# Kernel tuning notes

Hardware: AMD Instinct MI355X
Metric: run time of the kernel (lower is better)

The kernel has to match this reference:

```python
import jax, jax.numpy as jnp
import numpy as np

OUTPUT_BUDGET = 2048
PADDING_IDX = 0
BIG = 1e9
B, TG, M = 4, 32768, 4
N_ENT, N_REL, D = 100000, 512, 128
N_RULES = 64


def setup_inputs() -> dict:
    key = jax.random.key(0)
    ks = jax.random.split(key, 8)
    # entity ids in [1, N_ENT) so padding_idx=0 is reserved
    subj = jax.random.randint(ks[0], (B, TG, M), 1, N_ENT)
    pred = jax.random.randint(ks[1], (B, TG, M), 0, N_REL)
    obj = jax.random.randint(ks[2], (B, TG, M), 1, N_ENT)
    body = jnp.stack([subj, pred, obj], axis=-1)  # [B, TG, M, 3]
    pad = jax.random.uniform(ks[3], (B, TG, M)) < 0.25
    body = body.at[..., 0].set(jnp.where(pad, PADDING_IDX, body[..., 0]))
    mask = jax.random.uniform(ks[4], (B, TG)) < 0.9  # [B, TG] bool
    rule_idx = jax.random.randint(ks[5], (B, TG), 0, N_RULES)
    ent_emb = jax.random.normal(ks[6], (N_ENT, D), dtype=jnp.float32) * 0.1
    rel_emb = jax.random.normal(ks[7], (N_REL, D), dtype=jnp.float32) * 0.1
    return {"body": body, "mask": mask, "rule_idx": rule_idx,
            "ent_emb": ent_emb, "rel_emb": rel_emb}


def reference(body, mask, rule_idx, ent_emb, rel_emb):
    # KGE (DistMult) atom scoring: gather embeddings, tri-linear dot per atom
    s = ent_emb[body[..., 0]]   # [B, TG, M, D]
    r = rel_emb[body[..., 1]]   # [B, TG, M, D]
    o = ent_emb[body[..., 2]]   # [B, TG, M, D]
    atom_scores = jnp.einsum('btmd,btmd,btmd->btm', s, r, o)  # [B, TG, M]
    body_active = body[..., 0] != PADDING_IDX
    atom_scores = jnp.where(body_active, atom_scores, BIG)
    # min-conjunction over atoms, mask inactive groundings
    scores = jnp.min(atom_scores, axis=-1)            # [B, TG]
    scores = jnp.where(mask, scores, -BIG)
    # top-k select per batch row
    top_scores, top_idx = jax.lax.top_k(scores, OUTPUT_BUDGET)  # [B, K]
    body_sel = jnp.take_along_axis(body, top_idx[:, :, None, None], axis=1)  # [B, K, M, 3]
    mask_sel = jnp.take_along_axis(mask, top_idx, axis=1)        # [B, K]
    rule_sel = jnp.take_along_axis(rule_idx, top_idx, axis=1)    # [B, K]
    return body_sel, mask_sel, rule_sel, top_scores
```

## Files before the change

kernel.cpp:

```cpp
#include <hip/hip_runtime.h>
#include <hip/hip_bf16.h>
#include <hip/hip_fp16.h>
#include <stdint.h>

constexpr int B_    = 4;
constexpr int TG_   = 32768;
constexpr int D_    = 128;
constexpr int KOUT_ = 2048;
constexpr int NH_   = 4096;
constexpr int CAPL_ = 8192;
constexpr long ENTQ_ = 100000L * D_ / 4;
constexpr long RELQ_ = 512L * D_ / 4;
#define BIGF 1e9f

#define WS_KEYS(ws)   ((unsigned long long*)(ws))
#define WS_KEYS2(ws)  ((unsigned long long*)((char*)(ws) + (1u << 20)))
#define WS_GHIST(ws)  ((uint32_t*)((char*)(ws) + (2u << 20)))
#define WS_CHSCAN(ws) ((unsigned short*)((char*)(ws) + (2u << 20) + 65536u))
#define WS_REL8(ws)   ((unsigned char*)((char*)(ws) + (3u << 20)))
#define WS_ENT8(ws)   ((unsigned char*)((char*)(ws) + (3u << 20) + 65536u))

__device__ __forceinline__ uint32_t f2u_asc(float f) {
  uint32_t b = __float_as_uint(f);
  return (b & 0x80000000u) ? ~b : (b | 0x80000000u);
}
__device__ __forceinline__ float u2f_asc(uint32_t u) {
  uint32_t b = (u & 0x80000000u) ? (u & 0x7FFFFFFFu) : ~u;
  return __uint_as_float(b);
}

__device__ __forceinline__ bool mask_is_i32(const void* mask_raw) {
  const uint32_t* mw = (const uint32_t*)mask_raw;
  bool i32 = true;
  #pragma unroll
  for (int j = 0; j < 16; ++j) i32 &= (mw[j] <= 1u);
  return i32;
}
__device__ __forceinline__ int read_mask(const void* mask_raw, int idx, bool i32) {
  return i32 ? ((const int*)mask_raw)[idx]
             : (int)((const unsigned char*)mask_raw)[idx];
}

__device__ __forceinline__ uint32_t f2e5m2(float x) {
  uint32_t u = (uint32_t)__half_as_ushort(__float2half(x));
  return (u + 0x7Fu + ((u >> 8) & 1u)) >> 8;
}

__global__ __launch_bounds__(256) void convert_kernel(
    const float* __restrict__ ent, const float* __restrict__ rel,
    unsigned char* __restrict__ ent8, unsigned char* __restrict__ rel8) {
  long stride = (long)gridDim.x * 256;
  for (long q = (long)blockIdx.x * 256 + threadIdx.x; q < ENTQ_ + RELQ_; q += stride) {
    bool isEnt = (q < ENTQ_);
    long qq = isEnt ? q : (q - ENTQ_);
    float4 v = isEnt ? ((const float4*)ent)[qq] : ((const float4*)rel)[qq];
    uint32_t b = f2e5m2(v.x) | (f2e5m2(v.y) << 8) | (f2e5m2(v.z) << 16) | (f2e5m2(v.w) << 24);
    if (isEnt) ((uint32_t*)ent8)[qq] = b;
    else       ((uint32_t*)rel8)[qq] = b;
  }
}

__device__ __forceinline__ void expand4(uint32_t w, uint32_t& lo, uint32_t& hi) {
  lo = ((w << 8) & 0xFF00u)  | ((w << 16) & 0xFF000000u);
  hi = ((w >> 8) & 0xFF00u)  | (w & 0xFF000000u);
}

__device__ __forceinline__ float dot8_e5(uint32_t sx, uint32_t sy,
                                         uint32_t rx, uint32_t ry,
                                         uint32_t ox, uint32_t oy) {
  uint32_t sw[4], rw[4], ow[4];
  expand4(sx, sw[0], sw[1]); expand4(sy, sw[2], sw[3]);
  expand4(rx, rw[0], rw[1]); expand4(ry, rw[2], rw[3]);
  expand4(ox, ow[0], ow[1]); expand4(oy, ow[2], ow[3]);
  const __half2* sh = (const __half2*)sw;
  const __half2* rh = (const __half2*)rw;
  const __half2* oh = (const __half2*)ow;
  __half2 acc = __half2{__ushort_as_half(0), __ushort_as_half(0)};
  #pragma unroll
  for (int c = 0; c < 4; ++c)
    acc = __hfma2(__hmul2(sh[c], rh[c]), oh[c], acc);
  return __low2float(acc) + __high2float(acc);
}

__device__ __forceinline__ float dot16_e5(const uint4& s, const uint4& r, const uint4& o) {
  return dot8_e5(s.x, s.y, r.x, r.y, o.x, o.y)
       + dot8_e5(s.z, s.w, r.z, r.w, o.z, o.w);
}

__global__ __launch_bounds__(256, 4) void score_e5m2_kernel(
    const int* __restrict__ body, const void* __restrict__ mask,
    const unsigned char* __restrict__ ent8, const unsigned char* __restrict__ rel8,
    unsigned long long* __restrict__ keys, uint32_t* __restrict__ ghist) {
  if (blockIdx.x < 64) ghist[blockIdx.x * 256 + threadIdx.x] = 0;
  int lane = threadIdx.x & 63;
  int wv   = threadIdx.x >> 6;
  int wid0 = blockIdx.x * 32 + wv * 8;
  int g    = lane >> 3;
  int sl   = lane & 7;
  int wid  = wid0 + g;
  const uint4* bq = (const uint4*)(body + (long)wid * 12);
  uint4 b0 = bq[0], b1 = bq[1], b2 = bq[2];
  int sI[4] = {(int)b0.x, (int)b0.w, (int)b1.z, (int)b2.y};
  int rI[4] = {(int)b0.y, (int)b1.x, (int)b1.w, (int)b2.z};
  int oI[4] = {(int)b0.z, (int)b1.y, (int)b2.x, (int)b2.w};
  bool pd[4];
  #pragma unroll
  for (int a = 0; a < 4; ++a) {
    pd[a] = (sI[a] == 0);
    if (pd[a]) { rI[a] = 0; oI[a] = 0; }
  }
  uint4 S[4], R[4], O[4];
  #pragma unroll
  for (int a = 0; a < 4; ++a) {
    S[a] = ((const uint4*)(ent8 + (long)sI[a] * D_))[sl];
    R[a] = ((const uint4*)(rel8 + (long)rI[a] * D_))[sl];
    O[a] = ((const uint4*)(ent8 + (long)oI[a] * D_))[sl];
  }
  float q[4];
  #pragma unroll
  for (int a = 0; a < 4; ++a) q[a] = dot16_e5(S[a], R[a], O[a]);
  #pragma unroll
  for (int a = 0; a < 4; ++a) {
    q[a] += __shfl_xor(q[a], 1);
    q[a] += __shfl_xor(q[a], 2);
    q[a] += __shfl_xor(q[a], 4);
    q[a] = pd[a] ? BIGF : q[a];
  }
  float m = fminf(fminf(q[0], q[1]), fminf(q[2], q[3]));
  float sc = read_mask(mask, wid, mask_is_i32(mask)) ? m : -BIGF;
  if (sl == 0) {
    uint32_t dk = ~f2u_asc(sc);
    keys[wid] = ((unsigned long long)dk << 32) | (uint32_t)(wid & (TG_ - 1));
  }
}

__global__ __launch_bounds__(1024) void histsort_kernel(
    const unsigned long long* __restrict__ keys, uint32_t* __restrict__ ghist,
    unsigned short* __restrict__ chscan, unsigned long long* __restrict__ keys2) {
  __shared__ uint32_t lh[NH_];
  __shared__ uint32_t lb[NH_];
  __shared__ unsigned long long srt[2048];
  __shared__ uint32_t wexc[16];
  int row   = blockIdx.x >> 4;
  int chunk = blockIdx.x & 15;
  int tid = threadIdx.x, lane = tid & 63, wv = tid >> 6;
  const unsigned long long* kk = keys + (long)row * TG_ + chunk * 2048;
  #pragma unroll
  for (int i = 0; i < NH_ / 1024; ++i) { lh[tid + i*1024] = 0; lb[tid + i*1024] = 0; }
  __syncthreads();
  unsigned long long k0 = kk[tid], k1 = kk[tid + 1024];
  atomicAdd(&lh[(uint32_t)(k0 >> 52)], 1u);
  atomicAdd(&lh[(uint32_t)(k1 >> 52)], 1u);
  __syncthreads();
  uint32_t* gh = ghist + row * NH_;
  #pragma unroll
  for (int i = 0; i < NH_ / 1024; ++i) {
    uint32_t v = lh[tid + i * 1024];
    if (v) atomicAdd(&gh[tid + i * 1024], v);
  }
  uint32_t c0 = lh[4*tid], c1 = lh[4*tid+1], c2 = lh[4*tid+2], c3 = lh[4*tid+3];
  uint32_t s = c0 + c1 + c2 + c3;
  uint32_t inc = s;
  #pragma unroll
  for (int off = 1; off < 64; off <<= 1) {
    uint32_t t = __shfl_up(inc, off, 64);
    if (lane >= off) inc += t;
  }
  if (lane == 63) wexc[wv] = inc;
  __syncthreads();
  if (tid < 16) {
    uint32_t v = wexc[tid], iv = v;
    #pragma unroll
    for (int off = 1; off < 16; off <<= 1) {
      uint32_t t = __shfl_up(iv, off, 64);
      if (tid >= off) iv += t;
    }
    wexc[tid] = iv - v;
  }
  __syncthreads();
  uint32_t excl = wexc[wv] + inc - s;
  uint32_t e0 = excl, e1 = e0 + c0, e2 = e1 + c1, e3 = e2 + c2, incl = e3 + c3;
  unsigned short* gc = chscan + ((long)row * 16 + chunk) * NH_;
  ushort4 sv; sv.x = (unsigned short)e1; sv.y = (unsigned short)e2;
  sv.z = (unsigned short)e3; sv.w = (unsigned short)incl;
  ((ushort4*)gc)[tid] = sv;
  lh[4*tid] = e0; lh[4*tid+1] = e1; lh[4*tid+2] = e2; lh[4*tid+3] = e3;
  __syncthreads();
  uint32_t p0 = lh[(uint32_t)(k0 >> 52)] + atomicAdd(&lb[(uint32_t)(k0 >> 52)], 1u);
  srt[p0] = k0;
  uint32_t p1 = lh[(uint32_t)(k1 >> 52)] + atomicAdd(&lb[(uint32_t)(k1 >> 52)], 1u);
  srt[p1] = k1;
  __syncthreads();
  unsigned long long* k2 = keys2 + ((long)row * 16 + chunk) * 2048;
  ((uint4*)k2)[tid] = ((const uint4*)srt)[tid];
}

__global__ __launch_bounds__(1024) void finish_kernel(
    const unsigned long long* __restrict__ keys2, const uint32_t* __restrict__ ghist,
    const unsigned short* __restrict__ chscan,
    const int* __restrict__ body, const void* __restrict__ mask,
    const int* __restrict__ rule, float* __restrict__ out) {
  __shared__ uint32_t ofs[NH_];
  __shared__ uint32_t bofs[NH_];
  __shared__ unsigned long long cand[CAPL_];
  __shared__ uint32_t wexc[16];
  __shared__ uint32_t s_th;
  int tid  = threadIdx.x;
  int lane = tid & 63;
  int wv   = tid >> 6;
  int b    = blockIdx.x;
  const uint32_t* gh = ghist + b * NH_;
  uint4 cq = ((const uint4*)gh)[tid];
  uint32_t c0 = cq.x, c1 = cq.y, c2 = cq.z, c3 = cq.w;
  #pragma unroll
  for (int i = 0; i < NH_ / 1024; ++i) bofs[tid + i * 1024] = 0;
  uint32_t s = c0 + c1 + c2 + c3;
  uint32_t inc = s;
  #pragma unroll
  for (int off = 1; off < 64; off <<= 1) {
    uint32_t t = __shfl_up(inc, off, 64);
    if (lane >= off) inc += t;
  }
  if (lane == 63) wexc[wv] = inc;
  __syncthreads();
  if (tid < 16) {
    uint32_t v = wexc[tid], iv = v;
    #pragma unroll
    for (int off = 1; off < 16; off <<= 1) {
      uint32_t t = __shfl_up(iv, off, 64);
      if (tid >= off) iv += t;
    }
    wexc[tid] = iv - v;
  }
  __syncthreads();
  uint32_t excl = wexc[wv] + inc - s;
  uint32_t e0 = excl, e1 = e0 + c0, e2 = e1 + c1, e3 = e2 + c2, incl = e3 + c3;
  if (excl < (uint32_t)KOUT_ && incl >= (uint32_t)KOUT_) {
    uint32_t t4 = (uint32_t)tid * 4;
    s_th = (e1 >= (uint32_t)KOUT_) ? t4
         : (e2 >= (uint32_t)KOUT_) ? t4 + 1
         : (e3 >= (uint32_t)KOUT_) ? t4 + 2 : t4 + 3;
  }
  ofs[4*tid] = e0; ofs[4*tid+1] = e1; ofs[4*tid+2] = e2; ofs[4*tid+3] = e3;
  __syncthreads();
  uint32_t th = s_th;
  uint32_t cnt = (uint32_t)chscan[((long)b * 16 + wv) * NH_ + th];
  const unsigned long long* k2 = keys2 + ((long)b * 16 + wv) * 2048;
  for (uint32_t i = lane; i < cnt; i += 64) {
    unsigned long long key = k2[i];
    uint32_t pfx = (uint32_t)(key >> 52);
    uint32_t pos = ofs[pfx] + atomicAdd(&bofs[pfx], 1u);
    if (pos < (uint32_t)CAPL_) cand[pos] = key;
  }
  __syncthreads();
  uint32_t n = (th + 1 < (uint32_t)NH_) ? ofs[th + 1] : (uint32_t)TG_;
  if (n > (uint32_t)CAPL_) n = CAPL_;
  bool mi32 = mask_is_i32(mask);
  for (uint32_t slot = tid; slot < n; slot += 1024) {
    unsigned long long my = cand[slot];
    uint32_t pfx = (uint32_t)(my >> 52);
    uint32_t s0 = ofs[pfx];
    uint32_t s1 = (pfx + 1 < (uint32_t)NH_) ? ofs[pfx + 1] : n;
    if (s1 > n) s1 = n;
    uint32_t r = s0;
    for (uint32_t i = s0; i < s1; ++i) r += (cand[i] < my);
    if (r >= (uint32_t)KOUT_) continue;
    int t = (int)(my & 0xFFFFFFFFu);
    float sc = u2f_asc(~(uint32_t)(my >> 32));
    int g = b * TG_ + t;
    int idx = b * KOUT_ + (int)r;
    const int* at = body + (long)g * 12;
    float* ob = out + (long)idx * 12;
    #pragma unroll
    for (int c = 0; c < 12; ++c) ob[c] = (float)at[c];
    const int base1 = B_ * KOUT_ * 12;
    out[base1 + idx]                  = read_mask(mask, g, mi32) ? 1.0f : 0.0f;
    out[base1 + B_ * KOUT_ + idx]     = (float)rule[g];
    out[base1 + 2 * B_ * KOUT_ + idx] = sc;
  }
}

extern "C" void kernel_launch(void* const* d_in, const int* in_sizes, int n_in,
                              void* d_out, int out_size, void* d_ws, size_t ws_size,
                              hipStream_t stream) {
  const int*  body = (const int*)d_in[0];
  const void* mask = d_in[1];
  const int*  rule = (const int*)d_in[2];
  const float* ent = (const float*)d_in[3];
  const float* rel = (const float*)d_in[4];
  float* out = (float*)d_out;

  unsigned long long* keys  = WS_KEYS(d_ws);
  unsigned long long* keys2 = WS_KEYS2(d_ws);
  uint32_t*       ghist  = WS_GHIST(d_ws);
  unsigned short* chscan = WS_CHSCAN(d_ws);
  unsigned char*  ent8   = WS_ENT8(d_ws);
  unsigned char*  rel8   = WS_REL8(d_ws);

  convert_kernel<<<2048, 256, 0, stream>>>(ent, rel, ent8, rel8);
  score_e5m2_kernel<<<(B_ * TG_) / 32, 256, 0, stream>>>(body, mask, ent8, rel8, keys, ghist);
  histsort_kernel<<<B_ * 16, 1024, 0, stream>>>(keys, ghist, chscan, keys2);
  finish_kernel<<<B_, 1024, 0, stream>>>(keys2, ghist, chscan, body, mask, rule, out);
}
```

Measured before the change: 66.91 us.

## Fuse histogram sort and finish kernels using last-block completion counter

Merges the per-chunk histogram sort kernel and the per-row finish kernel into one launch. Each block bumps a per-row atomic counter after writing its sorted chunk, and the last block of each row runs the threshold selection and output gather. This removes one kernel launch and its dependency gap, at the cost of larger LDS use per block (the candidate buffer) and a threadfence/atomic handshake. The counter is reset in the scoring kernel.

After: 92.27 us. +37.9%, slower.

```diff
diff --git a/kernel.cpp b/kernel.cpp
--- a/kernel.cpp
+++ b/kernel.cpp
@@ -17,6 +17,7 @@
 #define WS_KEYS2(ws)  ((unsigned long long*)((char*)(ws) + (1u << 20)))
 #define WS_GHIST(ws)  ((uint32_t*)((char*)(ws) + (2u << 20)))
 #define WS_CHSCAN(ws) ((unsigned short*)((char*)(ws) + (2u << 20) + 65536u))
+#define WS_GDONE(ws)  ((uint32_t*)((char*)(ws) + (2u << 20) + 655360u))
 #define WS_REL8(ws)   ((unsigned char*)((char*)(ws) + (3u << 20)))
 #define WS_ENT8(ws)   ((unsigned char*)((char*)(ws) + (3u << 20) + 65536u))
 
@@ -90,8 +91,10 @@
 __global__ __launch_bounds__(256, 4) void score_e5m2_kernel(
     const int* __restrict__ body, const void* __restrict__ mask,
     const unsigned char* __restrict__ ent8, const unsigned char* __restrict__ rel8,
-    unsigned long long* __restrict__ keys, uint32_t* __restrict__ ghist) {
+    unsigned long long* __restrict__ keys, uint32_t* __restrict__ ghist,
+    uint32_t* __restrict__ gdone) {
   if (blockIdx.x < 64) ghist[blockIdx.x * 256 + threadIdx.x] = 0;
+  if (blockIdx.x == 64 && threadIdx.x < B_) gdone[threadIdx.x] = 0;
   int lane = threadIdx.x & 63;
   int wv   = threadIdx.x >> 6;
   int wid0 = blockIdx.x * 32 + wv * 8;
@@ -134,13 +137,18 @@
   }
 }
 
-__global__ __launch_bounds__(1024) void histsort_kernel(
+__global__ __launch_bounds__(1024) void histsort_finish_kernel(
     const unsigned long long* __restrict__ keys, uint32_t* __restrict__ ghist,
-    unsigned short* __restrict__ chscan, unsigned long long* __restrict__ keys2) {
+    unsigned short* __restrict__ chscan, unsigned long long* __restrict__ keys2,
+    uint32_t* __restrict__ gdone,
+    const int* __restrict__ body, const void* __restrict__ mask,
+    const int* __restrict__ rule, float* __restrict__ out) {
   __shared__ uint32_t lh[NH_];
   __shared__ uint32_t lb[NH_];
   __shared__ unsigned long long srt[2048];
+  __shared__ unsigned long long cand[CAPL_];
   __shared__ uint32_t wexc[16];
+  __shared__ uint32_t s_th, s_last;
   int row   = blockIdx.x >> 4;
   int chunk = blockIdx.x & 15;
   int tid = threadIdx.x, lane = tid & 63, wv = tid >> 6;
@@ -191,31 +199,22 @@
   uint32_t p1 = lh[(uint32_t)(k1 >> 52)] + atomicAdd(&lb[(uint32_t)(k1 >> 52)], 1u);
   srt[p1] = k1;
   __syncthreads();
-  unsigned long long* k2 = keys2 + ((long)row * 16 + chunk) * 2048;
-  ((uint4*)k2)[tid] = ((const uint4*)srt)[tid];
-}
-
-__global__ __launch_bounds__(1024) void finish_kernel(
-    const unsigned long long* __restrict__ keys2, const uint32_t* __restrict__ ghist,
-    const unsigned short* __restrict__ chscan,
-    const int* __restrict__ body, const void* __restrict__ mask,
-    const int* __restrict__ rule, float* __restrict__ out) {
-  __shared__ uint32_t ofs[NH_];
-  __shared__ uint32_t bofs[NH_];
-  __shared__ unsigned long long cand[CAPL_];
-  __shared__ uint32_t wexc[16];
-  __shared__ uint32_t s_th;
-  int tid  = threadIdx.x;
-  int lane = tid & 63;
-  int wv   = tid >> 6;
-  int b    = blockIdx.x;
-  const uint32_t* gh = ghist + b * NH_;
+  unsigned long long* k2o = keys2 + ((long)row * 16 + chunk) * 2048;
+  ((uint4*)k2o)[tid] = ((const uint4*)srt)[tid];
+
+  __threadfence();
+  __syncthreads();
+  if (tid == 0) s_last = (atomicAdd(&gdone[row], 1u) == 15u) ? 1u : 0u;
+  __syncthreads();
+  if (!s_last) return;
+  __threadfence();
+
+  #pragma unroll
+  for (int i = 0; i < NH_ / 1024; ++i) lb[tid + i * 1024] = 0;
   uint4 cq = ((const uint4*)gh)[tid];
-  uint32_t c0 = cq.x, c1 = cq.y, c2 = cq.z, c3 = cq.w;
-  #pragma unroll
-  for (int i = 0; i < NH_ / 1024; ++i) bofs[tid + i * 1024] = 0;
-  uint32_t s = c0 + c1 + c2 + c3;
-  uint32_t inc = s;
+  c0 = cq.x; c1 = cq.y; c2 = cq.z; c3 = cq.w;
+  s = c0 + c1 + c2 + c3;
+  inc = s;
   #pragma unroll
   for (int off = 1; off < 64; off <<= 1) {
     uint32_t t = __shfl_up(inc, off, 64);
@@ -233,42 +232,42 @@
     wexc[tid] = iv - v;
   }
   __syncthreads();
-  uint32_t excl = wexc[wv] + inc - s;
-  uint32_t e0 = excl, e1 = e0 + c0, e2 = e1 + c1, e3 = e2 + c2, incl = e3 + c3;
+  excl = wexc[wv] + inc - s;
+  e0 = excl; e1 = e0 + c0; e2 = e1 + c1; e3 = e2 + c2; incl = e3 + c3;
   if (excl < (uint32_t)KOUT_ && incl >= (uint32_t)KOUT_) {
     uint32_t t4 = (uint32_t)tid * 4;
     s_th = (e1 >= (uint32_t)KOUT_) ? t4
          : (e2 >= (uint32_t)KOUT_) ? t4 + 1
          : (e3 >= (uint32_t)KOUT_) ? t4 + 2 : t4 + 3;
   }
-  ofs[4*tid] = e0; ofs[4*tid+1] = e1; ofs[4*tid+2] = e2; ofs[4*tid+3] = e3;
+  lh[4*tid] = e0; lh[4*tid+1] = e1; lh[4*tid+2] = e2; lh[4*tid+3] = e3;
   __syncthreads();
   uint32_t th = s_th;
-  uint32_t cnt = (uint32_t)chscan[((long)b * 16 + wv) * NH_ + th];
-  const unsigned long long* k2 = keys2 + ((long)b * 16 + wv) * 2048;
+  uint32_t cnt = (uint32_t)chscan[((long)row * 16 + wv) * NH_ + th];
+  const unsigned long long* k2 = keys2 + ((long)row * 16 + wv) * 2048;
   for (uint32_t i = lane; i < cnt; i += 64) {
     unsigned long long key = k2[i];
     uint32_t pfx = (uint32_t)(key >> 52);
-    uint32_t pos = ofs[pfx] + atomicAdd(&bofs[pfx], 1u);
+    uint32_t pos = lh[pfx] + atomicAdd(&lb[pfx], 1u);
     if (pos < (uint32_t)CAPL_) cand[pos] = key;
   }
   __syncthreads();
-  uint32_t n = (th + 1 < (uint32_t)NH_) ? ofs[th + 1] : (uint32_t)TG_;
+  uint32_t n = (th + 1 < (uint32_t)NH_) ? lh[th + 1] : (uint32_t)TG_;
   if (n > (uint32_t)CAPL_) n = CAPL_;
   bool mi32 = mask_is_i32(mask);
   for (uint32_t slot = tid; slot < n; slot += 1024) {
     unsigned long long my = cand[slot];
     uint32_t pfx = (uint32_t)(my >> 52);
-    uint32_t s0 = ofs[pfx];
-    uint32_t s1 = (pfx + 1 < (uint32_t)NH_) ? ofs[pfx + 1] : n;
+    uint32_t s0 = lh[pfx];
+    uint32_t s1 = (pfx + 1 < (uint32_t)NH_) ? lh[pfx + 1] : n;
     if (s1 > n) s1 = n;
     uint32_t r = s0;
     for (uint32_t i = s0; i < s1; ++i) r += (cand[i] < my);
     if (r >= (uint32_t)KOUT_) continue;
     int t = (int)(my & 0xFFFFFFFFu);
     float sc = u2f_asc(~(uint32_t)(my >> 32));
-    int g = b * TG_ + t;
-    int idx = b * KOUT_ + (int)r;
+    int g = row * TG_ + t;
+    int idx = row * KOUT_ + (int)r;
     const int* at = body + (long)g * 12;
     float* ob = out + (long)idx * 12;
     #pragma unroll
@@ -294,11 +293,12 @@
   unsigned long long* keys2 = WS_KEYS2(d_ws);
   uint32_t*       ghist  = WS_GHIST(d_ws);
   unsigned short* chscan = WS_CHSCAN(d_ws);
+  uint32_t*       gdone  = WS_GDONE(d_ws);
   unsigned char*  ent8   = WS_ENT8(d_ws);
   unsigned char*  rel8   = WS_REL8(d_ws);
 
   convert_kernel<<<2048, 256, 0, stream>>>(ent, rel, ent8, rel8);
-  score_e5m2_kernel<<<(B_ * TG_) / 32, 256, 0, stream>>>(body, mask, ent8, rel8, keys, ghist);
-  histsort_kernel<<<B_ * 16, 1024, 0, stream>>>(keys, ghist, chscan, keys2);
-  finish_kernel<<<B_, 1024, 0, stream>>>(keys2, ghist, chscan, body, mask, rule, out);
-}
+  score_e5m2_kernel<<<(B_ * TG_) / 32, 256, 0, stream>>>(body, mask, ent8, rel8, keys, ghist, gdone);
+  histsort_finish_kernel<<<B_ * 16, 1024, 0, stream>>>(keys, ghist, chscan, keys2, gdone,
+                                                       body, mask, rule, out);
+}
```
